# Kernel optimization log

Measured on AMD Instinct MI355X. Metric: run time of the kernel, lower is better.

The kernel has to match this reference:

```python
import jax, jax.numpy as jnp
import numpy as np
import math


def _conv1x1(x, w, b):
    # x: [B,C,H,W], w: [O,C], b: [O] -> [B,O,H,W]
    return jnp.einsum('oc,bchw->bohw', w, x) + b[None, :, None, None]


def _attn_branch(x, f_w, f_b, g_w, g_b, h_w, h_b, gamma):
    B, C, H, W = x.shape
    N = H * W
    k_dim = C // 8
    f = _conv1x1(x, f_w, f_b).reshape(B, k_dim, N)  # [B,k,N]
    g = _conv1x1(x, g_w, g_b).reshape(B, k_dim, N)  # [B,k,N]
    # attention[b, n, m] = sum_k f[b,k,n] * g[b,k,m] / sqrt(k_dim)
    scores = jnp.einsum('bkn,bkm->bnm', f, g) / math.sqrt(k_dim)
    attn = jax.nn.softmax(scores, axis=2)  # softmax over last dim (dim=2)
    h = _conv1x1(x, h_w, h_b).reshape(B, C, N)  # [B,C,N]
    sa_map = jnp.einsum('bcn,bnm->bcm', h, attn).reshape(B, C, H, W)
    return gamma[0] * sa_map + x


def setup_inputs() -> dict:
    key = jax.random.key(0)
    ks = jax.random.split(key, 8)
    B, C, H, W = 4, 256, 64, 64
    kd = C // 8
    scale_in = 1.0 / math.sqrt(C)
    return {
        'x1': jax.random.normal(ks[0], (B, C, H, W), jnp.float32),
        'x2': jax.random.normal(ks[1], (B, C, H, W), jnp.float32),
        'f_w': jax.random.normal(ks[2], (kd, C), jnp.float32) * scale_in,
        'f_b': jnp.zeros((kd,), jnp.float32),
        'g_w': jax.random.normal(ks[3], (kd, C), jnp.float32) * scale_in,
        'g_b': jnp.zeros((kd,), jnp.float32),
        'h1_w': jax.random.normal(ks[4], (C, C), jnp.float32) * scale_in,
        'h1_b': jnp.zeros((C,), jnp.float32),
        'h2_w': jax.random.normal(ks[5], (C, C), jnp.float32) * scale_in,
        'h2_b': jnp.zeros((C,), jnp.float32),
        'gamma1': jax.random.normal(ks[6], (1,), jnp.float32),
        'gamma2': jax.random.normal(ks[7], (1,), jnp.float32),
    }


def reference(x1, x2, f_w, f_b, g_w, g_b, h1_w, h1_b, h2_w, h2_b, gamma1, gamma2):
    y1 = _attn_branch(x1, f_w, f_b, g_w, g_b, h1_w, h1_b, gamma1)
    y2 = _attn_branch(x2, f_w, f_b, g_w, g_b, h2_w, h2_b, gamma2)
    return (y1, y2)
```

## Files before the change

### kernel.cpp

```cpp
#include <hip/hip_runtime.h>
#include <math.h>

#define NDIM 4096
#define CDIM 256
#define KD   32
#define SCALE 0.17677669529663687f
#define SHIFT 8.0f

typedef __attribute__((ext_vector_type(8))) short short8;
typedef __attribute__((ext_vector_type(4))) float f32x4;
typedef unsigned short u16;
typedef unsigned int u32;

__device__ __forceinline__ u32 f2bf(float x) {
  union { float f; u32 u; } v; v.f = x;
  return (v.u + 0x7FFFu + ((v.u >> 16) & 1u)) >> 16;
}

#define MFMA16(a, b, c) __builtin_amdgcn_mfma_f32_16x16x32_bf16((a), (b), (c), 0, 0, 0)

__global__ void cast_bf16_kernel(const float* __restrict__ in,
                                 u16* __restrict__ out, int n) {
  int i = blockIdx.x * 256 + threadIdx.x;
  if (i < n) out[i] = (u16)f2bf(in[i]);
}

__global__ __launch_bounds__(256) void transpose_cast_kernel(
    const float* __restrict__ x1, const float* __restrict__ x2,
    u16* __restrict__ xt) {
  __shared__ float ts[64][68];
  const int t = threadIdx.x;
  const int ntile = blockIdx.x * 64, Ctile = blockIdx.y * 64, z = blockIdx.z;
  const float* xb = ((z >> 2) ? x2 : x1) + (size_t)(z & 3) * CDIM * NDIM;
  u16* xtb = xt + (size_t)z * NDIM * CDIM;
  const int r = t >> 4, c4 = (t & 15) * 4;
#pragma unroll
  for (int i = 0; i < 4; i++) {
    float4 v = *(const float4*)&xb[(size_t)(Ctile + r + i * 16) * NDIM + ntile + c4];
    *(float4*)&ts[r + i * 16][c4] = v;
  }
  __syncthreads();
  const int n = t >> 2, Cg = (t & 3) * 16;
  u32 pk[8];
#pragma unroll
  for (int j = 0; j < 8; j++) {
    u32 lo = f2bf(ts[Cg + 2 * j][n]);
    u32 hi = f2bf(ts[Cg + 2 * j + 1][n]);
    pk[j] = lo | (hi << 16);
  }
  uint4* dst = (uint4*)&xtb[(size_t)(ntile + n) * CDIM + Ctile + Cg];
  dst[0] = make_uint4(pk[0], pk[1], pk[2], pk[3]);
  dst[1] = make_uint4(pk[4], pk[5], pk[6], pk[7]);
}

__global__ __launch_bounds__(256) void conv_fg_kernel(
    const u16* __restrict__ W, const float* __restrict__ bias,
    const u16* __restrict__ xt, u16* __restrict__ outT) {
  const int t = threadIdx.x, w = t >> 6, l = t & 63, li = l & 15, q = l >> 4;
  const int ntile = blockIdx.x * 128, bb = blockIdx.y;
  const u16* xtb = xt + (size_t)bb * NDIM * CDIM;
  u16* ob = outT + (size_t)bb * NDIM * KD;
  f32x4 zero4 = {0.f, 0.f, 0.f, 0.f};
  f32x4 acc[2][2];
  for (int i = 0; i < 2; i++) for (int j = 0; j < 2; j++) acc[i][j] = zero4;

  for (int k0 = 0; k0 < CDIM; k0 += 32) {
    short8 a0 = *(const short8*)&W[(size_t)(li) * CDIM + k0 + q * 8];
    short8 a1 = *(const short8*)&W[(size_t)(16 + li) * CDIM + k0 + q * 8];
    short8 b0 = *(const short8*)&xtb[(size_t)(ntile + (w * 2) * 16 + li) * CDIM + k0 + q * 8];
    short8 b1 = *(const short8*)&xtb[(size_t)(ntile + (w * 2 + 1) * 16 + li) * CDIM + k0 + q * 8];
    acc[0][0] = MFMA16(a0, b0, acc[0][0]);
    acc[0][1] = MFMA16(a0, b1, acc[0][1]);
    acc[1][0] = MFMA16(a1, b0, acc[1][0]);
    acc[1][1] = MFMA16(a1, b1, acc[1][1]);
  }
#pragma unroll
  for (int os = 0; os < 2; os++) {
    float bv[4];
#pragma unroll
    for (int reg = 0; reg < 4; reg++) bv[reg] = bias[os * 16 + q * 4 + reg];
#pragma unroll
    for (int ns = 0; ns < 2; ns++) {
      int n = ntile + (w * 2 + ns) * 16 + li;
      u32 p0 = f2bf(acc[os][ns][0] + bv[0]) | (f2bf(acc[os][ns][1] + bv[1]) << 16);
      u32 p1 = f2bf(acc[os][ns][2] + bv[2]) | (f2bf(acc[os][ns][3] + bv[3]) << 16);
      *(uint2*)&ob[(size_t)n * KD + os * 16 + q * 4] = make_uint2(p0, p1);
    }
  }
}

__global__ __launch_bounds__(256) void conv_h_kernel(
    const u16* __restrict__ W, const float* __restrict__ bias,
    const u16* __restrict__ xt, u16* __restrict__ outH) {
  const int t = threadIdx.x, w = t >> 6, l = t & 63, li = l & 15, q = l >> 4;
  const int ntile = blockIdx.x * 64;
  const int o0 = blockIdx.y * 64 + w * 16;
  const int b = blockIdx.z;
  const u16* xtb = xt + (size_t)b * NDIM * CDIM;
  u16* ob = outH + (size_t)b * CDIM * NDIM;
  f32x4 zero4 = {0.f, 0.f, 0.f, 0.f};
  f32x4 acc[4];
  for (int i = 0; i < 4; i++) acc[i] = zero4;

  for (int k0 = 0; k0 < CDIM; k0 += 32) {
    short8 a = *(const short8*)&W[(size_t)(o0 + li) * CDIM + k0 + q * 8];
#pragma unroll
    for (int ns = 0; ns < 4; ns++) {
      short8 bf = *(const short8*)&xtb[(size_t)(ntile + ns * 16 + li) * CDIM + k0 + q * 8];
      acc[ns] = MFMA16(a, bf, acc[ns]);
    }
  }
  float bv[4];
#pragma unroll
  for (int reg = 0; reg < 4; reg++) bv[reg] = bias[o0 + q * 4 + reg];
#pragma unroll
  for (int ns = 0; ns < 4; ns++) {
    int n = ntile + ns * 16 + li;
#pragma unroll
    for (int reg = 0; reg < 4; reg++) {
      int c = o0 + q * 4 + reg;
      ob[(size_t)c * NDIM + n] = (u16)f2bf(acc[ns][reg] + bv[reg]);
    }
  }
}

__global__ __launch_bounds__(256) void stats_kernel(
    const u16* __restrict__ ft, const u16* __restrict__ gt,
    float* __restrict__ L) {
  __shared__ float zred[32][64];
  const int t = threadIdx.x, w = t >> 6, l = t & 63, li = l & 15, q = l >> 4;
  const int n0 = blockIdx.x * 32;
  const int bb = blockIdx.z * 4 + blockIdx.y;
  const u16* ftb = ft + (size_t)bb * NDIM * KD;
  const u16* gtb = gt + (size_t)bb * NDIM * KD;
  f32x4 zero4 = {0.f, 0.f, 0.f, 0.f};

  short8 a0 = *(const short8*)&ftb[(size_t)(n0 + li) * KD + q * 8];
  short8 a1 = *(const short8*)&ftb[(size_t)(n0 + 16 + li) * KD + q * 8];
  f32x4 z0 = zero4, z1 = zero4;

#pragma unroll 2
  for (int it = 0; it < 64; it++) {
    int m = (it * 4 + w) * 16;
    short8 bf = *(const short8*)&gtb[(size_t)(m + li) * KD + q * 8];
    f32x4 S0 = MFMA16(a0, bf, zero4);
    f32x4 S1 = MFMA16(a1, bf, zero4);
#pragma unroll
    for (int reg = 0; reg < 4; reg++) {
      z0[reg] += __expf(S0[reg] * SCALE - SHIFT);
      z1[reg] += __expf(S1[reg] * SCALE - SHIFT);
    }
  }
#pragma unroll
  for (int reg = 0; reg < 4; reg++) {
    zred[q * 4 + reg][w * 16 + li] = z0[reg];
    zred[16 + q * 4 + reg][w * 16 + li] = z1[reg];
  }
  __syncthreads();
  const int r = t >> 3, i8 = t & 7;
  float4 s1 = *(const float4*)&zred[r][i8 * 8];
  float4 s2 = *(const float4*)&zred[r][i8 * 8 + 4];
  float sum = s1.x + s1.y + s1.z + s1.w + s2.x + s2.y + s2.z + s2.w;
  sum += __shfl_xor(sum, 1, 8);
  sum += __shfl_xor(sum, 2, 8);
  sum += __shfl_xor(sum, 4, 8);
  if (i8 == 0) L[(size_t)bb * NDIM + n0 + r] = SHIFT + __logf(sum);
}

__global__ __launch_bounds__(512, 4) void apply_kernel(
    const u16* __restrict__ ft, const u16* __restrict__ gt,
    const u16* __restrict__ h, const float* __restrict__ L,
    const float* __restrict__ x1, const float* __restrict__ x2,
    const float* __restrict__ gamma1, const float* __restrict__ gamma2,
    float* __restrict__ out) {
  __shared__ u16 Pt[64][32];
  const int t = threadIdx.x, w = t >> 6, l = t & 63, li = l & 15, q = l >> 4;
  const int mtile = blockIdx.x * 64;
  const int b = blockIdx.y, br = blockIdx.z, bb = br * 4 + b;
  const u16* ftb = ft + (size_t)bb * NDIM * KD;
  const u16* gtb = gt + (size_t)bb * NDIM * KD;
  const u16* hb = h + (size_t)bb * CDIM * NDIM;
  const float* Lb = L + (size_t)bb * NDIM;
  const float* xb = (br ? x2 : x1) + (size_t)b * CDIM * NDIM;
  const float gmv = br ? gamma2[0] : gamma1[0];
  float* ob = out + (size_t)bb * CDIM * NDIM;

  const int nsub = w & 1, msub = w >> 1;
  const int c0 = w * 32;
  f32x4 zero4 = {0.f, 0.f, 0.f, 0.f};
  short8 gfrag = *(const short8*)&gtb[(size_t)(mtile + msub * 16 + li) * KD + q * 8];

  f32x4 acc[2][4];
  for (int i = 0; i < 2; i++) for (int j = 0; j < 4; j++) acc[i][j] = zero4;

  for (int n0 = 0; n0 < NDIM; n0 += 32) {
    short8 af = *(const short8*)&ftb[(size_t)(n0 + nsub * 16 + li) * KD + q * 8];
    f32x4 L4 = *(const f32x4*)&Lb[n0 + nsub * 16 + q * 4];
    short8 ah0 = *(const short8*)&hb[(size_t)(c0 + li) * NDIM + n0 + q * 8];
    short8 ah1 = *(const short8*)&hb[(size_t)(c0 + 16 + li) * NDIM + n0 + q * 8];

    f32x4 S = MFMA16(af, gfrag, zero4);
    u32 p0 = f2bf(__expf(S[0] * SCALE - L4[0])) |
             (f2bf(__expf(S[1] * SCALE - L4[1])) << 16);
    u32 p1 = f2bf(__expf(S[2] * SCALE - L4[2])) |
             (f2bf(__expf(S[3] * SCALE - L4[3])) << 16);

    __syncthreads();
    *(uint2*)&Pt[msub * 16 + li][nsub * 16 + q * 4] = make_uint2(p0, p1);
    __syncthreads();

#pragma unroll
    for (int ms = 0; ms < 4; ms++) {
      short8 bm = *(const short8*)&Pt[ms * 16 + li][q * 8];
      acc[0][ms] = MFMA16(ah0, bm, acc[0][ms]);
      acc[1][ms] = MFMA16(ah1, bm, acc[1][ms]);
    }
  }

#pragma unroll
  for (int cs = 0; cs < 2; cs++) {
#pragma unroll
    for (int ms = 0; ms < 4; ms++) {
#pragma unroll
      for (int reg = 0; reg < 4; reg++) {
        int c = c0 + cs * 16 + q * 4 + reg;
        int m = mtile + ms * 16 + li;
        size_t idx = (size_t)c * NDIM + m;
        ob[idx] = gmv * acc[cs][ms][reg] + xb[idx];
      }
    }
  }
}

extern "C" void kernel_launch(void* const* d_in, const int* in_sizes, int n_in,
                              void* d_out, int out_size, void* d_ws, size_t ws_size,
                              hipStream_t stream) {
  const float* x1 = (const float*)d_in[0];
  const float* x2 = (const float*)d_in[1];
  const float* f_w = (const float*)d_in[2];
  const float* f_b = (const float*)d_in[3];
  const float* g_w = (const float*)d_in[4];
  const float* g_b = (const float*)d_in[5];
  const float* h1_w = (const float*)d_in[6];
  const float* h1_b = (const float*)d_in[7];
  const float* h2_w = (const float*)d_in[8];
  const float* h2_b = (const float*)d_in[9];
  const float* gamma1 = (const float*)d_in[10];
  const float* gamma2 = (const float*)d_in[11];
  float* out = (float*)d_out;

  char* ws = (char*)d_ws;
  u16* xt  = (u16*)(ws);
  u16* wh  = (u16*)(ws + 16777216);
  u16* ftw = (u16*)(ws + 33554432);
  u16* gtw = (u16*)(ws + 35651584);
  u16* wWh = (u16*)(ws + 37748736);
  u16* wWf = (u16*)(ws + 38010880);
  u16* wWg = (u16*)(ws + 38027264);
  float* Lw = (float*)(ws + 38043648);

  cast_bf16_kernel<<<256, 256, 0, stream>>>(h1_w, wWh, 65536);
  cast_bf16_kernel<<<256, 256, 0, stream>>>(h2_w, wWh + 65536, 65536);
  cast_bf16_kernel<<<32, 256, 0, stream>>>(f_w, wWf, 8192);
  cast_bf16_kernel<<<32, 256, 0, stream>>>(g_w, wWg, 8192);

  transpose_cast_kernel<<<dim3(64, 4, 8), 256, 0, stream>>>(x1, x2, xt);

  conv_fg_kernel<<<dim3(32, 8), 256, 0, stream>>>(wWf, f_b, xt, ftw);
  conv_fg_kernel<<<dim3(32, 8), 256, 0, stream>>>(wWg, g_b, xt, gtw);
  conv_h_kernel<<<dim3(64, 4, 4), 256, 0, stream>>>(wWh, h1_b, xt, wh);
  conv_h_kernel<<<dim3(64, 4, 4), 256, 0, stream>>>(
      wWh + 65536, h2_b, xt + (size_t)4 * NDIM * CDIM, wh + (size_t)4 * CDIM * NDIM);

  stats_kernel<<<dim3(128, 4, 2), 256, 0, stream>>>(ftw, gtw, Lw);

  apply_kernel<<<dim3(64, 4, 2), 512, 0, stream>>>(ftw, gtw, wh, Lw, x1, x2,
                                                   gamma1, gamma2, out);
}
```

Baseline: 354.6 us.

## Merge launches and split apply kernel channels across twice as many blocks

Merges the four weight-cast launches into one and fuses the f and g 1x1 convs into a single kernel that reuses the x fragment. Also merges the two h conv launches into one grid covering both branches. The apply kernel now splits the 256 channels into two halves across blockIdx.y. This doubles the grid to 1024 blocks with fewer accumulators per wave and a higher occupancy hint. The cost is that the score/exp softmax work in apply is recomputed in each half, and the P tile gets padded rows.

Measured after the change: 395.6 us. 11.6% more time.

```diff
diff --git a/kernel.cpp b/kernel.cpp
--- a/kernel.cpp
+++ b/kernel.cpp
@@ -19,10 +19,18 @@
 
 #define MFMA16(a, b, c) __builtin_amdgcn_mfma_f32_16x16x32_bf16((a), (b), (c), 0, 0, 0)
 
-__global__ void cast_bf16_kernel(const float* __restrict__ in,
-                                 u16* __restrict__ out, int n) {
+__global__ void cast_all_kernel(const float* __restrict__ h1w,
+                                const float* __restrict__ h2w,
+                                const float* __restrict__ fw,
+                                const float* __restrict__ gw,
+                                u16* __restrict__ dst) {
   int i = blockIdx.x * 256 + threadIdx.x;
-  if (i < n) out[i] = (u16)f2bf(in[i]);
+  float v;
+  if (i < 65536) v = h1w[i];
+  else if (i < 131072) v = h2w[i - 65536];
+  else if (i < 139264) v = fw[i - 131072];
+  else v = gw[i - 139264];
+  dst[i] = (u16)f2bf(v);
 }
 
 __global__ __launch_bounds__(256) void transpose_cast_kernel(
@@ -54,50 +62,57 @@
 }
 
 __global__ __launch_bounds__(256) void conv_fg_kernel(
-    const u16* __restrict__ W, const float* __restrict__ bias,
-    const u16* __restrict__ xt, u16* __restrict__ outT) {
-  const int t = threadIdx.x, w = t >> 6, l = t & 63, li = l & 15, q = l >> 4;
-  const int ntile = blockIdx.x * 128, bb = blockIdx.y;
+    const u16* __restrict__ Wf, const float* __restrict__ fbias,
+    const u16* __restrict__ Wg, const float* __restrict__ gbias,
+    const u16* __restrict__ xt, u16* __restrict__ ftT, u16* __restrict__ gtT) {
+  const int t = threadIdx.x, w = t >> 6, l = t & 63, li = l & 15, q = l >> 4;
+  const int ntile = blockIdx.x * 64, bb = blockIdx.y;
   const u16* xtb = xt + (size_t)bb * NDIM * CDIM;
-  u16* ob = outT + (size_t)bb * NDIM * KD;
   f32x4 zero4 = {0.f, 0.f, 0.f, 0.f};
   f32x4 acc[2][2];
   for (int i = 0; i < 2; i++) for (int j = 0; j < 2; j++) acc[i][j] = zero4;
+  const int nrow = ntile + w * 16 + li;
 
   for (int k0 = 0; k0 < CDIM; k0 += 32) {
-    short8 a0 = *(const short8*)&W[(size_t)(li) * CDIM + k0 + q * 8];
-    short8 a1 = *(const short8*)&W[(size_t)(16 + li) * CDIM + k0 + q * 8];
-    short8 b0 = *(const short8*)&xtb[(size_t)(ntile + (w * 2) * 16 + li) * CDIM + k0 + q * 8];
-    short8 b1 = *(const short8*)&xtb[(size_t)(ntile + (w * 2 + 1) * 16 + li) * CDIM + k0 + q * 8];
-    acc[0][0] = MFMA16(a0, b0, acc[0][0]);
-    acc[0][1] = MFMA16(a0, b1, acc[0][1]);
-    acc[1][0] = MFMA16(a1, b0, acc[1][0]);
-    acc[1][1] = MFMA16(a1, b1, acc[1][1]);
-  }
-#pragma unroll
-  for (int os = 0; os < 2; os++) {
-    float bv[4];
-#pragma unroll
-    for (int reg = 0; reg < 4; reg++) bv[reg] = bias[os * 16 + q * 4 + reg];
-#pragma unroll
-    for (int ns = 0; ns < 2; ns++) {
-      int n = ntile + (w * 2 + ns) * 16 + li;
-      u32 p0 = f2bf(acc[os][ns][0] + bv[0]) | (f2bf(acc[os][ns][1] + bv[1]) << 16);
-      u32 p1 = f2bf(acc[os][ns][2] + bv[2]) | (f2bf(acc[os][ns][3] + bv[3]) << 16);
-      *(uint2*)&ob[(size_t)n * KD + os * 16 + q * 4] = make_uint2(p0, p1);
+    short8 bx = *(const short8*)&xtb[(size_t)nrow * CDIM + k0 + q * 8];
+    short8 af0 = *(const short8*)&Wf[(size_t)(li) * CDIM + k0 + q * 8];
+    short8 af1 = *(const short8*)&Wf[(size_t)(16 + li) * CDIM + k0 + q * 8];
+    short8 ag0 = *(const short8*)&Wg[(size_t)(li) * CDIM + k0 + q * 8];
+    short8 ag1 = *(const short8*)&Wg[(size_t)(16 + li) * CDIM + k0 + q * 8];
+    acc[0][0] = MFMA16(af0, bx, acc[0][0]);
+    acc[0][1] = MFMA16(af1, bx, acc[0][1]);
+    acc[1][0] = MFMA16(ag0, bx, acc[1][0]);
+    acc[1][1] = MFMA16(ag1, bx, acc[1][1]);
+  }
+  u16* outs[2] = {ftT + (size_t)bb * NDIM * KD, gtT + (size_t)bb * NDIM * KD};
+  const float* biases[2] = {fbias, gbias};
+#pragma unroll
+  for (int fg = 0; fg < 2; fg++) {
+#pragma unroll
+    for (int os = 0; os < 2; os++) {
+      float b0 = biases[fg][os * 16 + q * 4 + 0];
+      float b1 = biases[fg][os * 16 + q * 4 + 1];
+      float b2 = biases[fg][os * 16 + q * 4 + 2];
+      float b3 = biases[fg][os * 16 + q * 4 + 3];
+      u32 p0 = f2bf(acc[fg][os][0] + b0) | (f2bf(acc[fg][os][1] + b1) << 16);
+      u32 p1 = f2bf(acc[fg][os][2] + b2) | (f2bf(acc[fg][os][3] + b3) << 16);
+      *(uint2*)&outs[fg][(size_t)nrow * KD + os * 16 + q * 4] = make_uint2(p0, p1);
     }
   }
 }
 
 __global__ __launch_bounds__(256) void conv_h_kernel(
-    const u16* __restrict__ W, const float* __restrict__ bias,
-    const u16* __restrict__ xt, u16* __restrict__ outH) {
+    const u16* __restrict__ Wall, const float* __restrict__ b1,
+    const float* __restrict__ b2, const u16* __restrict__ xt,
+    u16* __restrict__ outH) {
   const int t = threadIdx.x, w = t >> 6, l = t & 63, li = l & 15, q = l >> 4;
   const int ntile = blockIdx.x * 64;
   const int o0 = blockIdx.y * 64 + w * 16;
-  const int b = blockIdx.z;
-  const u16* xtb = xt + (size_t)b * NDIM * CDIM;
-  u16* ob = outH + (size_t)b * CDIM * NDIM;
+  const int bb = blockIdx.z, branch = bb >> 2;
+  const u16* W = Wall + (size_t)branch * CDIM * CDIM;
+  const float* bias = branch ? b2 : b1;
+  const u16* xtb = xt + (size_t)bb * NDIM * CDIM;
+  u16* ob = outH + (size_t)bb * CDIM * NDIM;
   f32x4 zero4 = {0.f, 0.f, 0.f, 0.f};
   f32x4 acc[4];
   for (int i = 0; i < 4; i++) acc[i] = zero4;
@@ -167,16 +182,17 @@
   if (i8 == 0) L[(size_t)bb * NDIM + n0 + r] = SHIFT + __logf(sum);
 }
 
-__global__ __launch_bounds__(512, 4) void apply_kernel(
+__global__ __launch_bounds__(512, 8) void apply_kernel(
     const u16* __restrict__ ft, const u16* __restrict__ gt,
     const u16* __restrict__ h, const float* __restrict__ L,
     const float* __restrict__ x1, const float* __restrict__ x2,
     const float* __restrict__ gamma1, const float* __restrict__ gamma2,
     float* __restrict__ out) {
-  __shared__ u16 Pt[64][32];
+  __shared__ u16 Pt[64][40];
   const int t = threadIdx.x, w = t >> 6, l = t & 63, li = l & 15, q = l >> 4;
   const int mtile = blockIdx.x * 64;
-  const int b = blockIdx.y, br = blockIdx.z, bb = br * 4 + b;
+  const int b = blockIdx.y >> 1, ch = blockIdx.y & 1;
+  const int br = blockIdx.z, bb = br * 4 + b;
   const u16* ftb = ft + (size_t)bb * NDIM * KD;
   const u16* gtb = gt + (size_t)bb * NDIM * KD;
   const u16* hb = h + (size_t)bb * CDIM * NDIM;
@@ -186,18 +202,17 @@
   float* ob = out + (size_t)bb * CDIM * NDIM;
 
   const int nsub = w & 1, msub = w >> 1;
-  const int c0 = w * 32;
+  const int c0 = ch * 128 + w * 16;
   f32x4 zero4 = {0.f, 0.f, 0.f, 0.f};
   short8 gfrag = *(const short8*)&gtb[(size_t)(mtile + msub * 16 + li) * KD + q * 8];
 
-  f32x4 acc[2][4];
-  for (int i = 0; i < 2; i++) for (int j = 0; j < 4; j++) acc[i][j] = zero4;
+  f32x4 acc[4];
+  for (int j = 0; j < 4; j++) acc[j] = zero4;
 
   for (int n0 = 0; n0 < NDIM; n0 += 32) {
     short8 af = *(const short8*)&ftb[(size_t)(n0 + nsub * 16 + li) * KD + q * 8];
     f32x4 L4 = *(const f32x4*)&Lb[n0 + nsub * 16 + q * 4];
-    short8 ah0 = *(const short8*)&hb[(size_t)(c0 + li) * NDIM + n0 + q * 8];
-    short8 ah1 = *(const short8*)&hb[(size_t)(c0 + 16 + li) * NDIM + n0 + q * 8];
+    short8 ah = *(const short8*)&hb[(size_t)(c0 + li) * NDIM + n0 + q * 8];
 
     f32x4 S = MFMA16(af, gfrag, zero4);
     u32 p0 = f2bf(__expf(S[0] * SCALE - L4[0])) |
@@ -212,22 +227,18 @@
 #pragma unroll
     for (int ms = 0; ms < 4; ms++) {
       short8 bm = *(const short8*)&Pt[ms * 16 + li][q * 8];
-      acc[0][ms] = MFMA16(ah0, bm, acc[0][ms]);
-      acc[1][ms] = MFMA16(ah1, bm, acc[1][ms]);
-    }
-  }
-
-#pragma unroll
-  for (int cs = 0; cs < 2; cs++) {
-#pragma unroll
-    for (int ms = 0; ms < 4; ms++) {
-#pragma unroll
-      for (int reg = 0; reg < 4; reg++) {
-        int c = c0 + cs * 16 + q * 4 + reg;
-        int m = mtile + ms * 16 + li;
-        size_t idx = (size_t)c * NDIM + m;
-        ob[idx] = gmv * acc[cs][ms][reg] + xb[idx];
-      }
+      acc[ms] = MFMA16(ah, bm, acc[ms]);
+    }
+  }
+
+#pragma unroll
+  for (int ms = 0; ms < 4; ms++) {
+#pragma unroll
+    for (int reg = 0; reg < 4; reg++) {
+      int c = c0 + q * 4 + reg;
+      int m = mtile + ms * 16 + li;
+      size_t idx = (size_t)c * NDIM + m;
+      ob[idx] = gmv * acc[ms][reg] + xb[idx];
     }
   }
 }
@@ -259,21 +270,15 @@
   u16* wWg = (u16*)(ws + 38027264);
   float* Lw = (float*)(ws + 38043648);
 
-  cast_bf16_kernel<<<256, 256, 0, stream>>>(h1_w, wWh, 65536);
-  cast_bf16_kernel<<<256, 256, 0, stream>>>(h2_w, wWh + 65536, 65536);
-  cast_bf16_kernel<<<32, 256, 0, stream>>>(f_w, wWf, 8192);
-  cast_bf16_kernel<<<32, 256, 0, stream>>>(g_w, wWg, 8192);
+  cast_all_kernel<<<576, 256, 0, stream>>>(h1_w, h2_w, f_w, g_w, wWh);
 
   transpose_cast_kernel<<<dim3(64, 4, 8), 256, 0, stream>>>(x1, x2, xt);
 
-  conv_fg_kernel<<<dim3(32, 8), 256, 0, stream>>>(wWf, f_b, xt, ftw);
-  conv_fg_kernel<<<dim3(32, 8), 256, 0, stream>>>(wWg, g_b, xt, gtw);
-  conv_h_kernel<<<dim3(64, 4, 4), 256, 0, stream>>>(wWh, h1_b, xt, wh);
-  conv_h_kernel<<<dim3(64, 4, 4), 256, 0, stream>>>(
-      wWh + 65536, h2_b, xt + (size_t)4 * NDIM * CDIM, wh + (size_t)4 * CDIM * NDIM);
+  conv_fg_kernel<<<dim3(64, 8), 256, 0, stream>>>(wWf, f_b, wWg, g_b, xt, ftw, gtw);
+  conv_h_kernel<<<dim3(64, 4, 8), 256, 0, stream>>>(wWh, h1_b, h2_b, xt, wh);
 
   stats_kernel<<<dim3(128, 4, 2), 256, 0, stream>>>(ftw, gtw, Lw);
 
-  apply_kernel<<<dim3(64, 4, 2), 512, 0, stream>>>(ftw, gtw, wh, Lw, x1, x2,
+  apply_kernel<<<dim3(64, 8, 2), 512, 0, stream>>>(ftw, gtw, wh, Lw, x1, x2,
                                                    gamma1, gamma2, out);
 }
```
